# Kernel tuning notes

Measured on AMD Instinct MI355X. Metric: run time of the kernel, lower is better.

## Reference

```python
import jax, jax.numpy as jnp
import numpy as np

# Static module config (matches init_kwargs)
K = 9            # kernel_size for piecewise-linear basis with kernel_shape (3,4)
GROUPS = 1
NLAT_IN, NLON_IN = 361, 720
NLAT_OUT, NLON_OUT = 181, 360
NNZ = 120000


def _disco_s2_contraction(x, ker_idx, row_idx, col_idx, vals):
    """Sparse DISCO contraction: y[b,c,k,ho,wo] = sum_e [ker_e=k][row_e=ho]
    vals_e * x[b,c,hi_e,(wi_e + wo*pscale) % nlon_in].
    Implemented as a longitude-roll scan with gather + segment_sum (no dense psi)."""
    B, C, Hi, Wi = x.shape
    pscale = Wi // NLON_OUT
    hi = col_idx // Wi          # [nnz] input latitude
    wi = col_idx % Wi           # [nnz] input longitude (unshifted)
    seg = ker_idx * NLAT_OUT + row_idx  # [nnz] output (k, ho) segment id

    def step(x_c, _):
        # gather all nnz entries for the current longitude shift: [nnz, B*C]
        g = x_c[:, :, hi, wi].reshape(B * C, -1).T
        y = jax.ops.segment_sum(g * vals[:, None], seg, num_segments=K * NLAT_OUT)
        # roll so next output longitude sees x[..., (wi + pscale) % Wi]
        return jnp.roll(x_c, -pscale, axis=-1), y

    _, ys = jax.lax.scan(step, x, None, length=NLON_OUT)  # [Wo, K*Ho, B*C]
    y = jnp.transpose(ys, (2, 1, 0)).reshape(B, C, K, NLAT_OUT, NLON_OUT)
    return y


def setup_inputs() -> dict:
    key = jax.random.key(0)
    k1, k2, k3, k4, k5, k6, k7 = jax.random.split(key, 7)
    B, Cin, Cout = 1, 32, 32
    x = jax.random.normal(k1, (B, Cin, NLAT_IN, NLON_IN), dtype=jnp.float32)
    psi_ker_idx = jax.random.randint(k2, (NNZ,), 0, K)
    psi_row_idx = jax.random.randint(k3, (NNZ,), 0, NLAT_OUT)
    psi_col_idx = jax.random.randint(k4, (NNZ,), 0, NLAT_IN * NLON_IN)
    psi_vals = jax.random.normal(k5, (NNZ,), dtype=jnp.float32) * 0.05
    groupsize = Cin // GROUPS
    scale = np.sqrt(1.0 / groupsize)
    weight = scale * jax.random.normal(k6, (Cout, groupsize, K), dtype=jnp.float32)
    bias = jax.random.normal(k7, (Cout,), dtype=jnp.float32) * 0.01
    return {"x": x, "psi_ker_idx": psi_ker_idx, "psi_row_idx": psi_row_idx,
            "psi_col_idx": psi_col_idx, "psi_vals": psi_vals,
            "weight": weight, "bias": bias}


def reference(x, psi_ker_idx, psi_row_idx, psi_col_idx, psi_vals, weight, bias):
    # sparse gather-weight-scatter contraction -> [B, C, K, Ho, Wo]
    xk = _disco_s2_contraction(x, psi_ker_idx, psi_row_idx, psi_col_idx, psi_vals)
    B, C, _, H, W = xk.shape
    groupsize = C // GROUPS
    xk = xk.reshape(B, GROUPS, groupsize, K, H, W)
    w = weight.reshape(GROUPS, -1, weight.shape[1], weight.shape[2])  # [g, o, c, k]
    out = jnp.einsum('bgckxy,gock->bgoxy', xk, w).reshape(B, -1, H, W)
    out = out + bias.reshape(1, -1, 1, 1)
    return out
```

## Files before the change

### kernel.cpp

```cpp
#include <hip/hip_runtime.h>
#include <hip/hip_bf16.h>
#include <stdint.h>

typedef uint32_t u32;
typedef unsigned short u16;
typedef float v2f __attribute__((ext_vector_type(2)));

#define NLAT_I 361
#define NLON_I 720
#define NLAT_O 181
#define NLON_O 360
#define KK 9
#define NNZ 120000
#define NSEG (KK * NLAT_O)
#define NPIX (NLAT_O * NLON_O)
#define NCH 32
#define ROWLEN 5760

#define NBLK1 233
#define SEGS_PER_BLK 7
#define NC 4
#define CAP 320
#define SPIN_LIMIT 100

#define PACK_BLKS ((NNZ + 255) / 256)

__device__ __forceinline__ u32 f2bf_rne(float f) {
    u32 b = __float_as_uint(f);
    return (b + 0x7FFFu + ((b >> 16) & 1u)) >> 16;
}

__device__ __forceinline__ int imin(int a, int b) { return a < b ? a : b; }

__global__ __launch_bounds__(256) void front_kernel(const float* __restrict__ x,
                                                    u32* __restrict__ xp,
                                                    const int* __restrict__ ker,
                                                    const int* __restrict__ row,
                                                    const int* __restrict__ col,
                                                    const float* __restrict__ vals,
                                                    int2* __restrict__ recs2,
                                                    int* __restrict__ ctr) {
    int tid = threadIdx.x;
    if (blockIdx.x >= NLAT_I) {
        int pb = blockIdx.x - NLAT_I;
        if (pb == 0 && tid < 16) ctr[tid] = 0;
        int e = pb * 256 + tid;
        if (e < NNZ) {
            int seg = ker[e] * NLAT_O + row[e];
            int c = col[e];
            int hi = c / NLON_I;
            int wi = c - hi * NLON_I;
            int p = wi & 1;
            int a = wi >> 1;
            u32 key = ((u32)seg << 19) | ((u32)hi << 10) | ((u32)p << 9) | (u32)a;
            recs2[e] = make_int2((int)key, __float_as_int(vals[e]));
        }
        return;
    }
    __shared__ u16 tile[32][732];
    int hi = blockIdx.x;
    const size_t plane = (size_t)NLAT_I * NLON_I;
#pragma unroll 1
    for (int c = 0; c < NCH; c++) {
        for (int cl = tid; cl < NLON_I; cl += 256) {
            tile[c][cl] = (u16)f2bf_rne(x[c * plane + (size_t)hi * NLON_I + cl]);
        }
    }
    __syncthreads();
    for (int wdx = tid; wdx < 2 * ROWLEN; wdx += 256) {
        int p = wdx / ROWLEN;
        int rem = wdx - p * ROWLEN;
        int j = rem >> 4;
        int cp = rem & 15;
        int cl = 2 * j + p;
        u32 v = (u32)tile[2 * cp][cl] | ((u32)tile[2 * cp + 1][cl] << 16);
        xp[(size_t)(2 * hi + p) * ROWLEN + rem] = v;
    }
}


__device__ __forceinline__ v2f bf2(u32 u) {
    v2f r;
    r.x = __uint_as_float(u << 16);
    r.y = __uint_as_float(u & 0xFFFF0000u);
    return r;
}

__device__ __forceinline__ const uint4* entry_ptr(const u32* __restrict__ xph,
                                                  u32 m, int w) {
    int row = (int)(m >> 9);
    int a   = (int)(m & 0x1FF);
    int idx = a + w;
    idx = (idx >= NLON_O) ? idx - NLON_O : idx;
    return (const uint4*)(xph + ((size_t)(row * NLON_O + idx) << 4));
}

#define FMA8(q0, q1, vv, A)                 \
    {                                       \
        A[0] = bf2(q0.x) * vv + A[0];       \
        A[1] = bf2(q0.y) * vv + A[1];       \
        A[2] = bf2(q0.z) * vv + A[2];       \
        A[3] = bf2(q0.w) * vv + A[3];       \
        A[4] = bf2(q1.x) * vv + A[4];       \
        A[5] = bf2(q1.y) * vv + A[5];       \
        A[6] = bf2(q1.z) * vv + A[6];       \
        A[7] = bf2(q1.w) * vv + A[7];       \
    }

__device__ __forceinline__ void proc_range(const u32* __restrict__ xph,
                                           const int2* __restrict__ rec,
                                           int beg, int end, int w,
                                           v2f* __restrict__ A) {
    int i = beg;
#pragma unroll 1
    for (; i + 4 <= end; i += 4) {
        int2 r0 = rec[i];
        int2 r1 = rec[i + 1];
        int2 r2 = rec[i + 2];
        int2 r3 = rec[i + 3];
        const uint4* p0 = entry_ptr(xph, (u32)r0.x, w);
        const uint4* p1 = entry_ptr(xph, (u32)r1.x, w);
        const uint4* p2 = entry_ptr(xph, (u32)r2.x, w);
        const uint4* p3 = entry_ptr(xph, (u32)r3.x, w);
        uint4 a0 = p0[0]; uint4 a1 = p0[1];
        uint4 b0 = p1[0]; uint4 b1 = p1[1];
        uint4 c0 = p2[0]; uint4 c1 = p2[1];
        uint4 d0 = p3[0]; uint4 d1 = p3[1];
        v2f v0 = {__int_as_float(r0.y), __int_as_float(r0.y)};
        v2f v1 = {__int_as_float(r1.y), __int_as_float(r1.y)};
        v2f v2 = {__int_as_float(r2.y), __int_as_float(r2.y)};
        v2f v3 = {__int_as_float(r3.y), __int_as_float(r3.y)};
        FMA8(a0, a1, v0, A)
        FMA8(b0, b1, v1, A)
        FMA8(c0, c1, v2, A)
        FMA8(d0, d1, v3, A)
    }
#pragma unroll 1
    for (; i < end; ++i) {
        int2 r0 = rec[i];
        const uint4* p0 = entry_ptr(xph, (u32)r0.x, w);
        uint4 a0 = p0[0]; uint4 a1 = p0[1];
        v2f v0 = {__int_as_float(r0.y), __int_as_float(r0.y)};
        FMA8(a0, a1, v0, A)
    }
}

__global__ __launch_bounds__(768, 3) void stage1_kernel(const u32* __restrict__ xp,
                                                        const int2* __restrict__ recs2,
                                                        int* __restrict__ ctr,
                                                        u16* __restrict__ xk) {
    __shared__ int2 lrec[SEGS_PER_BLK][CAP];
    __shared__ int lcnt[8];

    int b = blockIdx.x;
    int tid = threadIdx.x;
    int base = b * SEGS_PER_BLK;

    if (tid < 8) lcnt[tid] = 0;
    __syncthreads();

#pragma unroll 4
    for (int e = tid; e < NNZ; e += 768) {
        int2 r = recs2[e];
        int seg = (int)(((u32)r.x) >> 19);
        unsigned rel = (unsigned)(seg - base);
        if (rel < (unsigned)SEGS_PER_BLK) {
            int pos = atomicAdd(&lcnt[rel], 1);
            if (pos < CAP)
                lrec[rel][pos] = make_int2((int)(((u32)r.x) & 0x7FFFFu), r.y);
        }
    }
    __syncthreads();

#pragma unroll 1
    for (int slot = 0; slot < SEGS_PER_BLK; slot++) {
        int cnt = imin(lcnt[slot], CAP);
        int2 myrec;
        int myrank = -1;
        if (tid < cnt) {
            myrec = lrec[slot][tid];
            u32 k = (u32)myrec.x;
            int rank = 0;
            for (int j = 0; j < cnt; j++) {
                u32 kj = (u32)lrec[slot][j].x;
                rank += (kj < k || (kj == k && j < tid)) ? 1 : 0;
            }
            myrank = rank;
        }
        __syncthreads();
        if (myrank >= 0) lrec[slot][myrank] = myrec;
    }
    __syncthreads();

    int wo = tid >> 1, h = tid & 1;
    bool act = wo < NLON_O;
    int w = act ? wo : 0;
    const u32* xph = xp + h * 8;

    v2f acc[SEGS_PER_BLK][8];
#pragma unroll
    for (int slot = 0; slot < SEGS_PER_BLK; slot++)
#pragma unroll
        for (int j = 0; j < 8; j++) acc[slot][j] = (v2f){0.0f, 0.0f};

    for (int c = 0; c < NC; c++) {
#pragma unroll
        for (int slot = 0; slot < SEGS_PER_BLK; slot++) {
            int cnt = imin(lcnt[slot], CAP);
            int beg = (c * cnt) / NC;
            int end = ((c + 1) * cnt) / NC;
            proc_range(xph, lrec[slot], beg, end, w, acc[slot]);
        }
        if (c < NC - 1) {
            __syncthreads();
            if (tid == 0) {
                __hip_atomic_fetch_add(&ctr[c], 1, __ATOMIC_RELAXED,
                                       __HIP_MEMORY_SCOPE_AGENT);
                int spins = 0;
                while (spins < SPIN_LIMIT &&
                       __hip_atomic_load(&ctr[c], __ATOMIC_RELAXED,
                                         __HIP_MEMORY_SCOPE_AGENT) < (int)gridDim.x) {
                    __builtin_amdgcn_s_sleep(2);
                    ++spins;
                }
            }
            __syncthreads();
        }
    }

    if (act) {
#pragma unroll
        for (int slot = 0; slot < SEGS_PER_BLK; slot++) {
            int s = base + slot;
            if (s < NSEG) {
                int k = s / NLAT_O;
                int ho = s - k * NLAT_O;
                int pix = ho * NLON_O + wo;
#pragma unroll
                for (int j = 0; j < 8; j++) {
                    int ch = h * 16 + 2 * j;
                    xk[(size_t)(ch * KK + k) * NPIX + pix] =
                        (u16)f2bf_rne(acc[slot][j].x);
                    xk[(size_t)((ch + 1) * KK + k) * NPIX + pix] =
                        (u16)f2bf_rne(acc[slot][j].y);
                }
            }
        }
    }
}

#define S2_PP 64
#define S2_RPK 72

__global__ __launch_bounds__(256) void stage2_kernel(const u16* __restrict__ xk,
                                                     const float* __restrict__ W,
                                                     const float* __restrict__ bias,
                                                     float* __restrict__ out) {
    __shared__ float2 red[4][S2_PP][17];
    int pp  = threadIdx.x & 63;
    int ksl = threadIdx.x >> 6;
    int px2 = blockIdx.x * S2_PP + pp;
    bool act = px2 < NPIX / 2;
    int px = act ? px2 : 0;
    const u32* xk32 = (const u32*)xk;

    float a0[NCH], a1[NCH];
#pragma unroll
    for (int o = 0; o < NCH; o++) { a0[o] = 0.0f; a1[o] = 0.0f; }

    int rbase = ksl * S2_RPK;
#pragma unroll 4
    for (int rr = 0; rr < S2_RPK; rr++) {
        int r = rbase + rr;
        u32 u = xk32[(size_t)r * (NPIX / 2) + px];
        float x0 = __uint_as_float(u << 16);
        float x1 = __uint_as_float(u & 0xFFFF0000u);
#pragma unroll
        for (int o = 0; o < NCH; o++) {
            float wv = W[o * (NCH * KK) + r];
            a0[o] = fmaf(wv, x0, a0[o]);
            a1[o] = fmaf(wv, x1, a1[o]);
        }
    }

#pragma unroll 1
    for (int half = 0; half < 2; half++) {
        __syncthreads();
#pragma unroll
        for (int j = 0; j < 16; j++) {
            int o = half * 16 + j;
            red[ksl][pp][j] = make_float2(a0[o], a1[o]);
        }
        __syncthreads();
#pragma unroll
        for (int j = 0; j < 4; j++) {
            int oo = ksl * 4 + j;
            float2 s0 = red[0][pp][oo];
            float2 s1 = red[1][pp][oo];
            float2 s2 = red[2][pp][oo];
            float2 s3 = red[3][pp][oo];
            float sx = s0.x + s1.x + s2.x + s3.x;
            float sy = s0.y + s1.y + s2.y + s3.y;
            int o = half * 16 + oo;
            if (act) {
                float bv = bias[o];
                float2 v = make_float2(sx + bv, sy + bv);
                *(float2*)(out + (size_t)o * NPIX + 2 * px2) = v;
            }
        }
    }
}

extern "C" void kernel_launch(void* const* d_in, const int* in_sizes, int n_in,
                              void* d_out, int out_size, void* d_ws, size_t ws_size,
                              hipStream_t stream) {
    const float* x    = (const float*)d_in[0];
    const int* ker    = (const int*)d_in[1];
    const int* row    = (const int*)d_in[2];
    const int* col    = (const int*)d_in[3];
    const float* vals = (const float*)d_in[4];
    const float* W    = (const float*)d_in[5];
    const float* bias = (const float*)d_in[6];
    float* out        = (float*)d_out;

    char* ws = (char*)d_ws;
    const size_t off_xp  = 0;
    const size_t sz_xp   = (size_t)NLAT_I * 2 * ROWLEN * 4;
    const size_t off_ctr = off_xp + sz_xp;
    const size_t off_rec = off_ctr + 64;
    const size_t off_xk  = off_rec + (size_t)NNZ * 8;

    u32* xp    = (u32*)(ws + off_xp);
    int* ctr   = (int*)(ws + off_ctr);
    int2* recs2 = (int2*)(ws + off_rec);
    u16* xk    = (u16*)(ws + off_xk);

    front_kernel<<<NLAT_I + PACK_BLKS, 256, 0, stream>>>(x, xp, ker, row, col,
                                                         vals, recs2, ctr);
    stage1_kernel<<<NBLK1, 768, 0, stream>>>(xp, recs2, ctr, xk);
    stage2_kernel<<<(NPIX / 2 + S2_PP - 1) / S2_PP, 256, 0, stream>>>(xk, W, bias, out);
}
```

Before: 344.1 us.

## Pre-bin sparse records per stage1 block using global atomics in front kernel

The front kernel now scatters each nonzero into a per-block bin via a global atomic counter, storing a segment-relative key. Each stage1 block then reads only its own bin instead of all 120k records being scanned by every one of 233 blocks. This removes a large redundant global read and filter pass, at the cost of global atomics, a memset launch, and a fixed bin capacity that could drop records if it overflows.

```diff
diff --git a/kernel.cpp b/kernel.cpp
--- a/kernel.cpp
+++ b/kernel.cpp
@@ -21,6 +21,7 @@
 #define SEGS_PER_BLK 7
 #define NC 4
 #define CAP 320
+#define BINCAP 1024
 #define SPIN_LIMIT 100
 
 #define PACK_BLKS ((NNZ + 255) / 256)
@@ -38,22 +39,24 @@
                                                     const int* __restrict__ row,
                                                     const int* __restrict__ col,
                                                     const float* __restrict__ vals,
-                                                    int2* __restrict__ recs2,
-                                                    int* __restrict__ ctr) {
+                                                    int* __restrict__ bincnt,
+                                                    int2* __restrict__ binrec) {
     int tid = threadIdx.x;
     if (blockIdx.x >= NLAT_I) {
-        int pb = blockIdx.x - NLAT_I;
-        if (pb == 0 && tid < 16) ctr[tid] = 0;
-        int e = pb * 256 + tid;
+        int e = (blockIdx.x - NLAT_I) * 256 + tid;
         if (e < NNZ) {
             int seg = ker[e] * NLAT_O + row[e];
+            int blk = seg / SEGS_PER_BLK;
+            int rel = seg - blk * SEGS_PER_BLK;
             int c = col[e];
             int hi = c / NLON_I;
             int wi = c - hi * NLON_I;
             int p = wi & 1;
             int a = wi >> 1;
-            u32 key = ((u32)seg << 19) | ((u32)hi << 10) | ((u32)p << 9) | (u32)a;
-            recs2[e] = make_int2((int)key, __float_as_int(vals[e]));
+            u32 key = ((u32)rel << 19) | ((u32)hi << 10) | ((u32)p << 9) | (u32)a;
+            int pos = atomicAdd(&bincnt[blk], 1);
+            if (pos < BINCAP)
+                binrec[blk * BINCAP + pos] = make_int2((int)key, __float_as_int(vals[e]));
         }
         return;
     }
@@ -88,7 +91,7 @@
 
 __device__ __forceinline__ const uint4* entry_ptr(const u32* __restrict__ xph,
                                                   u32 m, int w) {
-    int row = (int)(m >> 9);
+    int row = (int)((m >> 9) & 0x3FFu);
     int a   = (int)(m & 0x1FF);
     int idx = a + w;
     idx = (idx >= NLON_O) ? idx - NLON_O : idx;
@@ -146,7 +149,8 @@
 }
 
 __global__ __launch_bounds__(768, 3) void stage1_kernel(const u32* __restrict__ xp,
-                                                        const int2* __restrict__ recs2,
+                                                        const int* __restrict__ bincnt,
+                                                        const int2* __restrict__ binrec,
                                                         int* __restrict__ ctr,
                                                         u16* __restrict__ xk) {
     __shared__ int2 lrec[SEGS_PER_BLK][CAP];
@@ -159,16 +163,14 @@
     if (tid < 8) lcnt[tid] = 0;
     __syncthreads();
 
-#pragma unroll 4
-    for (int e = tid; e < NNZ; e += 768) {
-        int2 r = recs2[e];
-        int seg = (int)(((u32)r.x) >> 19);
-        unsigned rel = (unsigned)(seg - base);
-        if (rel < (unsigned)SEGS_PER_BLK) {
-            int pos = atomicAdd(&lcnt[rel], 1);
-            if (pos < CAP)
-                lrec[rel][pos] = make_int2((int)(((u32)r.x) & 0x7FFFFu), r.y);
-        }
+    int bcnt = imin(bincnt[b], BINCAP);
+    const int2* mybin = binrec + b * BINCAP;
+    for (int e = tid; e < bcnt; e += 768) {
+        int2 r = mybin[e];
+        int rel = (int)(((u32)r.x) >> 19);
+        int pos = atomicAdd(&lcnt[rel], 1);
+        if (pos < CAP)
+            lrec[rel][pos] = make_int2((int)(((u32)r.x) & 0x7FFFFu), r.y);
     }
     __syncthreads();
 
@@ -324,19 +326,23 @@
     float* out        = (float*)d_out;
 
     char* ws = (char*)d_ws;
-    const size_t off_xp  = 0;
-    const size_t sz_xp   = (size_t)NLAT_I * 2 * ROWLEN * 4;
-    const size_t off_ctr = off_xp + sz_xp;
-    const size_t off_rec = off_ctr + 64;
-    const size_t off_xk  = off_rec + (size_t)NNZ * 8;
-
-    u32* xp    = (u32*)(ws + off_xp);
-    int* ctr   = (int*)(ws + off_ctr);
-    int2* recs2 = (int2*)(ws + off_rec);
-    u16* xk    = (u16*)(ws + off_xk);
+    const size_t off_xp   = 0;
+    const size_t sz_xp    = (size_t)NLAT_I * 2 * ROWLEN * 4;
+    const size_t off_ctr  = off_xp + sz_xp;
+    const size_t off_bcnt = off_ctr + 64;
+    const size_t off_bin  = off_bcnt + 1024;
+    const size_t off_xk   = off_bin + (size_t)NBLK1 * BINCAP * 8;
+
+    u32* xp      = (u32*)(ws + off_xp);
+    int* ctr     = (int*)(ws + off_ctr);
+    int* bincnt  = (int*)(ws + off_bcnt);
+    int2* binrec = (int2*)(ws + off_bin);
+    u16* xk      = (u16*)(ws + off_xk);
+
+    hipMemsetAsync(ws + off_ctr, 0, 64 + 1024, stream);
 
     front_kernel<<<NLAT_I + PACK_BLKS, 256, 0, stream>>>(x, xp, ker, row, col,
-                                                         vals, recs2, ctr);
-    stage1_kernel<<<NBLK1, 768, 0, stream>>>(xp, recs2, ctr, xk);
+                                                         vals, bincnt, binrec);
+    stage1_kernel<<<NBLK1, 768, 0, stream>>>(xp, bincnt, binrec, ctr, xk);
     stage2_kernel<<<(NPIX / 2 + S2_PP - 1) / S2_PP, 256, 0, stream>>>(xk, W, bias, out);
 }
```

New measurement: 365.9 us. 6.3% more time.
